# Kernel optimization log

Measured on AMD Instinct MI355X. Metric: run time of the kernel, lower is better.

The kernel has to match this reference:

```python
import jax, jax.numpy as jnp
import numpy as np

DIM = 512
HEADS = 8


def setup_inputs() -> dict:
    key = jax.random.key(0)
    k1, k2, k3, k4 = jax.random.split(key, 4)
    head_dim = DIM // HEADS
    scale = head_dim ** -0.5
    x = jax.random.normal(k1, (4, 4096, DIM), dtype=jnp.float32)
    Wqkv = jax.random.normal(k2, (3 * DIM, DIM), dtype=jnp.float32) * (DIM ** -0.5)
    temperature = jnp.ones((HEADS, 1, 1), dtype=jnp.float32) * scale
    Wproj = jax.random.normal(k3, (DIM, DIM), dtype=jnp.float32) * (DIM ** -0.5)
    bproj = jnp.zeros((DIM,), dtype=jnp.float32)
    return {"x": x, "Wqkv": Wqkv, "temperature": temperature, "Wproj": Wproj, "bproj": bproj}


def reference(x, Wqkv, temperature, Wproj, bproj):
    B, N, C = x.shape
    H = temperature.shape[0]
    D = C // H
    qkv = (x @ Wqkv.T).reshape(B, N, 3, H, D).transpose(2, 0, 3, 1, 4)  # (3,B,H,N,D)
    q, k, v = qkv[0], qkv[1], qkv[2]
    q = jax.nn.relu(q)
    k = jax.nn.relu(k)
    # denom = clamp(q @ sum_n k, min=100) -> (B,H,N,1)
    ksum = k.sum(axis=2)  # (B,H,D)
    denom = jnp.clip(jnp.einsum('bhnd,bhd->bhn', q, ksum), 100.0)[..., None]
    # attn = (k^T v) * temperature -> (B,H,D,D)
    attn = jnp.einsum('bhnd,bhne->bhde', k, v) * temperature
    attn1 = jnp.einsum('bhnd,bhde->bhne', q, attn)  # (B,H,N,D)
    out = attn1 / denom
    y = out.transpose(0, 2, 1, 3).reshape(B, N, C) @ Wproj.T + bproj
    return (y, attn1)
```

## Files before the change

### kernel.cpp

```cpp
#include <hip/hip_runtime.h>
#include <cstdint>
#include <cstddef>

typedef _Float16 f16;
typedef _Float16 f16x4 __attribute__((ext_vector_type(4)));
typedef _Float16 f16x8 __attribute__((ext_vector_type(8)));
typedef float f32x4 __attribute__((ext_vector_type(4)));
typedef __fp16 h2 __attribute__((ext_vector_type(2)));

#define MFMA16(a, b, c) __builtin_amdgcn_mfma_f32_16x16x32_f16(a, b, c, 0, 0, 0)

static __device__ __forceinline__ void gld16(const void* g, void* l) {
  __builtin_amdgcn_global_load_lds(
      (const __attribute__((address_space(1))) void*)g,
      (__attribute__((address_space(3))) void*)l, 16, 0, 0);
}

static __device__ __forceinline__ h2 as_h2(uint32_t u) {
  union { uint32_t u; h2 h; } c; c.u = u; return c.h;
}

#define B_ 4
#define N_ 4096
#define C_ 512
#define H_ 8
#define D_ 64
#define BN_ROWS 16384
#define QKV_COLS 1536

__global__ __launch_bounds__(256) void k_convert(
    const float* __restrict__ x, const float* __restrict__ wqkv,
    const float* __restrict__ wproj,
    f16* __restrict__ xh, f16* __restrict__ wqkvh, f16* __restrict__ wprojh)
{
  const int NX  = (BN_ROWS * C_) / 4;
  const int NW1 = (QKV_COLS * C_) / 4;
  const int NW2 = (C_ * C_) / 4;
  const int total = NX + NW1 + NW2;
  const int stride = gridDim.x * blockDim.x;
  for (int i = blockIdx.x * blockDim.x + threadIdx.x; i < total; i += stride) {
    const float4* s; f16x4* d; int j;
    if (i < NX)              { s = (const float4*)x;     d = (f16x4*)xh;     j = i; }
    else if (i < NX + NW1)   { s = (const float4*)wqkv;  d = (f16x4*)wqkvh;  j = i - NX; }
    else                     { s = (const float4*)wproj; d = (f16x4*)wprojh; j = i - NX - NW1; }
    float4 v = s[j];
    f16x4 o; o[0] = (f16)v.x; o[1] = (f16)v.y; o[2] = (f16)v.z; o[3] = (f16)v.w;
    d[j] = o;
  }
}

__global__ __launch_bounds__(256) void k_qkv_gemm(
    const f16* __restrict__ X, const f16* __restrict__ W, f16* __restrict__ Out)
{
  __shared__ f16 As[128][64];
  __shared__ f16 Bs[128][64];
  int w = (blockIdx.x & 7) * 192 + (blockIdx.x >> 3);
  const int n0 = (w % 12) * 128;
  const int m0 = (w / 12) * 128;
  const int tid = threadIdx.x;
  const int wid = tid >> 6;
  const int lane = tid & 63;
  const int lr = lane & 15, lg = lane >> 4;
  const int sr = lane >> 3;
  const int sslot = (lane & 7) ^ sr;
  const int wr = (wid >> 1) * 64, wc = (wid & 1) * 64;
  f32x4 acc[4][4] = {};
  for (int kt = 0; kt < 512; kt += 64) {
#pragma unroll
    for (int i = 0; i < 4; ++i) {
      int chunk = wid * 4 + i;
      int row = chunk * 8 + sr;
      gld16(&X[(size_t)(m0 + row) * 512 + kt + sslot * 8], &As[chunk * 8][0]);
      gld16(&W[(size_t)(n0 + row) * 512 + kt + sslot * 8], &Bs[chunk * 8][0]);
    }
    __syncthreads();
#pragma unroll
    for (int kk = 0; kk < 2; ++kk) {
      f16x8 af[4], bf[4];
#pragma unroll
      for (int m = 0; m < 4; ++m)
        af[m] = *(const f16x8*)&As[wr + m * 16 + lr][(((kk * 4 + lg) ^ (lr & 7)) * 8)];
#pragma unroll
      for (int n = 0; n < 4; ++n)
        bf[n] = *(const f16x8*)&Bs[wc + n * 16 + lr][(((kk * 4 + lg) ^ (lr & 7)) * 8)];
#pragma unroll
      for (int m = 0; m < 4; ++m)
#pragma unroll
        for (int n = 0; n < 4; ++n)
          acc[m][n] = MFMA16(bf[n], af[m], acc[m][n]);
    }
    __syncthreads();
  }
#pragma unroll
  for (int m = 0; m < 4; ++m)
#pragma unroll
    for (int n = 0; n < 4; ++n) {
      int row = m0 + wr + m * 16 + lr;
      int col = n0 + wc + n * 16 + lg * 4;
      f16x4 o;
      bool relu = (col < 1024);
#pragma unroll
      for (int j = 0; j < 4; ++j) {
        float v = acc[m][n][j];
        if (relu) v = fmaxf(v, 0.f);
        o[j] = (f16)v;
      }
      *(f16x4*)&Out[(size_t)row * QKV_COLS + col] = o;
    }
}

__global__ __launch_bounds__(256) void k_ktv(
    const f16* __restrict__ qkv, float* __restrict__ partial, float* __restrict__ pksum)
{
  __shared__ f16 ks[32][64];
  __shared__ f16 vs[32][64];
  const int bh = blockIdx.x, sp = blockIdx.y;
  const int b = bh >> 3, h = bh & 7;
  const int tid = threadIdx.x, wid = tid >> 6, lane = tid & 63;
  const int srow = lane >> 3, scol = (lane & 7) * 8;
  const int td = (wid << 2) | (lane >> 4);
  const int te = lane & 15;
  const uint32_t SEL_LO = 0x05040100u, SEL_HI = 0x07060302u;
  const h2 ones = {(__fp16)1.0f, (__fp16)1.0f};
  float acc[4][4] = {};
  float ksacc[4] = {0.f, 0.f, 0.f, 0.f};
  const size_t rowbase = (size_t)b * N_ + sp * 256;
  for (int t = 0; t < 8; ++t) {
    int nb = t * 32 + wid * 8 + srow;
    gld16(&qkv[(rowbase + nb) * QKV_COLS + 512 + h * 64 + scol], &ks[wid * 8][0]);
    gld16(&qkv[(rowbase + nb) * QKV_COLS + 1024 + h * 64 + scol], &vs[wid * 8][0]);
    __syncthreads();
#pragma unroll 4
    for (int n = 0; n < 32; n += 2) {
      uint2 ka = *(const uint2*)&ks[n][td * 4];
      uint2 kb = *(const uint2*)&ks[n + 1][td * 4];
      uint2 va = *(const uint2*)&vs[n][te * 4];
      uint2 vb = *(const uint2*)&vs[n + 1][te * 4];
      uint32_t kp[4], vp[4];
      kp[0] = __builtin_amdgcn_perm(kb.x, ka.x, SEL_LO);
      kp[1] = __builtin_amdgcn_perm(kb.x, ka.x, SEL_HI);
      kp[2] = __builtin_amdgcn_perm(kb.y, ka.y, SEL_LO);
      kp[3] = __builtin_amdgcn_perm(kb.y, ka.y, SEL_HI);
      vp[0] = __builtin_amdgcn_perm(vb.x, va.x, SEL_LO);
      vp[1] = __builtin_amdgcn_perm(vb.x, va.x, SEL_HI);
      vp[2] = __builtin_amdgcn_perm(vb.y, va.y, SEL_LO);
      vp[3] = __builtin_amdgcn_perm(vb.y, va.y, SEL_HI);
#pragma unroll
      for (int i = 0; i < 4; ++i)
#pragma unroll
        for (int j = 0; j < 4; ++j)
          acc[i][j] = __builtin_amdgcn_fdot2(as_h2(kp[i]), as_h2(vp[j]), acc[i][j], false);
      if (te == 0) {
#pragma unroll
        for (int i = 0; i < 4; ++i)
          ksacc[i] = __builtin_amdgcn_fdot2(as_h2(kp[i]), ones, ksacc[i], false);
      }
    }
    __syncthreads();
  }
  float* pp = partial + (size_t)(bh * 16 + sp) * 4096;
#pragma unroll
  for (int i = 0; i < 4; ++i)
#pragma unroll
    for (int j = 0; j < 4; ++j)
      pp[(td * 4 + i) * 64 + te * 4 + j] = acc[i][j];
  if (te == 0) {
    float* kp2 = pksum + (bh * 16 + sp) * 64;
#pragma unroll
    for (int i = 0; i < 4; ++i) kp2[td * 4 + i] = ksacc[i];
  }
}

__global__ __launch_bounds__(256) void k_reduce(
    const float* __restrict__ partial, const float* __restrict__ pksum,
    float* __restrict__ attn_acc, float* __restrict__ ksum)
{
  const int bh = blockIdx.x, seg = blockIdx.y, tid = threadIdx.x;
  const int i = seg * 256 + tid;
  float s = 0.f;
#pragma unroll 8
  for (int sp = 0; sp < 16; ++sp) s += partial[(size_t)(bh * 16 + sp) * 4096 + i];
  attn_acc[bh * 4096 + i] = s;
  if (seg == 0 && tid < 64) {
    float t2 = 0.f;
#pragma unroll 8
    for (int sp = 0; sp < 16; ++sp) t2 += pksum[(bh * 16 + sp) * 64 + tid];
    ksum[bh * 64 + tid] = t2;
  }
}

__global__ __launch_bounds__(512, 1) void k_attn_proj(
    const f16* __restrict__ qkv, const float* __restrict__ attn_acc,
    const float* __restrict__ ksum, const float* __restrict__ temp,
    const f16* __restrict__ Wp, const float* __restrict__ bias,
    float* __restrict__ attn1_out, float* __restrict__ Y)
{
  __shared__ f16 outs[8][64][64];
  __shared__ union {
    f16 attnT[8][64][64];
    f16 Bs[512][64];
  } u;
  __shared__ float ksum_s[512];
  __shared__ float bias_s[512];
  __shared__ float denom_s[8][64];

  const int bid = blockIdx.x;
  const int b = bid >> 6, sp = bid & 63;
  const size_t gr = (size_t)b * N_ + sp * 64;
  const int tid = threadIdx.x;
  const int wid = tid >> 6, lane = tid & 63;
  const int lr = lane & 15, lg = lane >> 4;
  const int sr = lane >> 3, sslot = (lane & 7) ^ sr;

  ksum_s[tid] = ksum[b * 512 + tid];
  bias_s[tid] = bias[tid];
  __syncthreads();

  {
    const int h = wid;
    const float tsc = temp[h];
#pragma unroll
    for (int rr = 0; rr < 8; ++rr)
      gld16(&qkv[(gr + rr * 8 + sr) * QKV_COLS + h * 64 + sslot * 8],
            &outs[h][rr * 8][0]);
#pragma unroll
    for (int dc = 0; dc < 4; ++dc) {
      float vals[16];
#pragma unroll
      for (int x = 0; x < 16; ++x)
        vals[x] = attn_acc[(size_t)(b * 8 + h) * 4096 + (dc * 16 + x) * 64 + lane] * tsc;
#pragma unroll
      for (int half = 0; half < 2; ++half) {
        int slot = (dc * 2 + half) ^ (lane & 7);
        f16x8 pk;
#pragma unroll
        for (int j = 0; j < 8; ++j) pk[j] = (f16)vals[half * 8 + j];
        *(f16x8*)&u.attnT[h][lane][slot * 8] = pk;
      }
    }
    asm volatile("s_waitcnt vmcnt(0)" ::: "memory");
    {
      const int r = lane;
      float dot = 0.f;
#pragma unroll
      for (int c = 0; c < 8; ++c) {
        f16x8 qv = *(const f16x8*)&outs[h][r][((c ^ (r & 7)) * 8)];
#pragma unroll
        for (int j = 0; j < 8; ++j) dot += (float)qv[j] * ksum_s[h * 64 + c * 8 + j];
      }
      denom_s[h][r] = fmaxf(dot, 100.f);
    }
    f16x8 af[2][4], bf[4][2];
#pragma unroll
    for (int kk = 0; kk < 2; ++kk)
#pragma unroll
      for (int m = 0; m < 4; ++m)
        af[kk][m] = *(const f16x8*)&outs[h][m * 16 + lr][(((kk * 4 + lg) ^ (lr & 7)) * 8)];
#pragma unroll
    for (int et = 0; et < 4; ++et)
#pragma unroll
      for (int kk = 0; kk < 2; ++kk)
        bf[et][kk] = *(const f16x8*)&u.attnT[h][et * 16 + lr][(((kk * 4 + lg) ^ (lr & 7)) * 8)];
    f32x4 acc1[4][4] = {};
#pragma unroll
    for (int kk = 0; kk < 2; ++kk)
#pragma unroll
      for (int m = 0; m < 4; ++m)
#pragma unroll
        for (int et = 0; et < 4; ++et)
          acc1[m][et] = MFMA16(bf[et][kk], af[kk][m], acc1[m][et]);
#pragma unroll
    for (int m = 0; m < 4; ++m) {
      const int rl = m * 16 + lr;
      const float dn = denom_s[h][rl];
#pragma unroll
      for (int et = 0; et < 4; ++et) {
        int e = et * 16 + lg * 4;
        float4 o;
        o.x = acc1[m][et][0]; o.y = acc1[m][et][1]; o.z = acc1[m][et][2]; o.w = acc1[m][et][3];
        *(float4*)&attn1_out[((size_t)(b * 8 + h) * N_ + sp * 64 + rl) * 64 + e] = o;
        f16x4 oh;
#pragma unroll
        for (int j = 0; j < 4; ++j) oh[j] = (f16)(acc1[m][et][j] / dn);
        *(f16x4*)((char*)&outs[h][rl][0] + (((e >> 3) ^ (rl & 7)) * 16) + (lg & 1) * 8) = oh;
      }
    }
  }
  __syncthreads();

  f32x4 accP[4][4] = {};
  for (int kc = 0; kc < 8; ++kc) {
#pragma unroll
    for (int rd = 0; rd < 8; ++rd)
      gld16(&Wp[(size_t)(wid * 64 + rd * 8 + sr) * 512 + kc * 64 + sslot * 8],
            &u.Bs[wid * 64 + rd * 8][0]);
    __syncthreads();
    f16x8 afp[2][4];
#pragma unroll
    for (int kk = 0; kk < 2; ++kk)
#pragma unroll
      for (int m = 0; m < 4; ++m)
        afp[kk][m] = *(const f16x8*)&outs[kc][m * 16 + lr][(((kk * 4 + lg) ^ (lr & 7)) * 8)];
#pragma unroll
    for (int kk = 0; kk < 2; ++kk) {
      f16x8 bfp[4];
#pragma unroll
      for (int n = 0; n < 4; ++n)
        bfp[n] = *(const f16x8*)&u.Bs[wid * 64 + n * 16 + lr][(((kk * 4 + lg) ^ (lr & 7)) * 8)];
#pragma unroll
      for (int m = 0; m < 4; ++m)
#pragma unroll
        for (int n = 0; n < 4; ++n)
          accP[m][n] = MFMA16(bfp[n], afp[kk][m], accP[m][n]);
    }
    __syncthreads();
  }

#pragma unroll
  for (int m = 0; m < 4; ++m)
#pragma unroll
    for (int n = 0; n < 4; ++n) {
      size_t row = gr + m * 16 + lr;
      int col = wid * 64 + n * 16 + lg * 4;
      float4 o;
      o.x = accP[m][n][0] + bias_s[col + 0];
      o.y = accP[m][n][1] + bias_s[col + 1];
      o.z = accP[m][n][2] + bias_s[col + 2];
      o.w = accP[m][n][3] + bias_s[col + 3];
      *(float4*)&Y[row * C_ + col] = o;
    }
}

extern "C" void kernel_launch(void* const* d_in, const int* in_sizes, int n_in,
                              void* d_out, int out_size, void* d_ws, size_t ws_size,
                              hipStream_t stream)
{
  const float* x     = (const float*)d_in[0];
  const float* wqkv  = (const float*)d_in[1];
  const float* temp  = (const float*)d_in[2];
  const float* wproj = (const float*)d_in[3];
  const float* bproj = (const float*)d_in[4];
  float* y_out     = (float*)d_out;
  float* attn1_out = (float*)d_out + 8388608;

  char* ws = (char*)d_ws;
  f16*   xh       = (f16*)(ws);
  float* partial  = (float*)(ws);
  f16*   wqkvh    = (f16*)(ws + 16777216);
  f16*   wprojh   = (f16*)(ws + 18350080);
  f16*   qkvh     = (f16*)(ws + 18874368);
  float* attn_acc = (float*)(ws + 69206016);
  float* ksum     = (float*)(ws + 69730304);
  float* pksum    = (float*)(ws + 69738496);

  hipLaunchKernelGGL(k_convert,   dim3(2048),   dim3(256), 0, stream, x, wqkv, wproj, xh, wqkvh, wprojh);
  hipLaunchKernelGGL(k_qkv_gemm,  dim3(1536),   dim3(256), 0, stream, xh, wqkvh, qkvh);
  hipLaunchKernelGGL(k_ktv,       dim3(32, 16), dim3(256), 0, stream, qkvh, partial, pksum);
  hipLaunchKernelGGL(k_reduce,    dim3(32, 16), dim3(256), 0, stream, partial, pksum, attn_acc, ksum);
  hipLaunchKernelGGL(k_attn_proj, dim3(256),    dim3(512), 0, stream,
                     qkvh, attn_acc, ksum, temp, wprojh, bproj, attn1_out, y_out);
}
```

Measured before the change: 107.4 us.

## Prefetch per-wave Wproj tiles early and drop block barriers in projection loop

The projection GEMM's Wproj tile loads now target LDS regions that only the issuing wave reads, so the per-iteration __syncthreads pairs become per-wave vmcnt/lgkmcnt waits. The next k-chunk is prefetched right after the current fragments are in registers. The first chunk is staged before the attn1 MFMAs, reusing the wave's own attnT slot in the union. s_setprio is raised around the MFMA bursts. This is meant to hide global-load latency and barrier stalls, but it depends on exact LDS aliasing and hand-placed waitcnts.

```diff
diff --git a/kernel.cpp b/kernel.cpp
--- a/kernel.cpp
+++ b/kernel.cpp
@@ -216,6 +216,14 @@
   bias_s[tid] = bias[tid];
   __syncthreads();
 
+#define STAGEPB(kc_)                                                          \
+  do {                                                                        \
+    _Pragma("unroll")                                                         \
+    for (int rd = 0; rd < 8; ++rd)                                            \
+      gld16(&Wp[(size_t)(wid * 64 + rd * 8 + sr) * 512 + (kc_) * 64 + sslot * 8], \
+            &u.Bs[wid * 64 + rd * 8][0]);                                     \
+  } while (0)
+
   {
     const int h = wid;
     const float tsc = temp[h];
@@ -261,7 +269,11 @@
 #pragma unroll
       for (int kk = 0; kk < 2; ++kk)
         bf[et][kk] = *(const f16x8*)&u.attnT[h][et * 16 + lr][(((kk * 4 + lg) ^ (lr & 7)) * 8)];
+    asm volatile("s_waitcnt lgkmcnt(0)" ::: "memory");
+    __builtin_amdgcn_sched_barrier(0);
+    STAGEPB(0);
     f32x4 acc1[4][4] = {};
+    __builtin_amdgcn_s_setprio(1);
 #pragma unroll
     for (int kk = 0; kk < 2; ++kk)
 #pragma unroll
@@ -269,6 +281,7 @@
 #pragma unroll
         for (int et = 0; et < 4; ++et)
           acc1[m][et] = MFMA16(bf[et][kk], af[kk][m], acc1[m][et]);
+    __builtin_amdgcn_s_setprio(0);
 #pragma unroll
     for (int m = 0; m < 4; ++m) {
       const int rl = m * 16 + lr;
@@ -286,35 +299,38 @@
       }
     }
   }
-  __syncthreads();
+  asm volatile("s_waitcnt lgkmcnt(0)" ::: "memory");
+  __builtin_amdgcn_s_barrier();
+  asm volatile("" ::: "memory");
 
   f32x4 accP[4][4] = {};
+#pragma unroll
   for (int kc = 0; kc < 8; ++kc) {
-#pragma unroll
-    for (int rd = 0; rd < 8; ++rd)
-      gld16(&Wp[(size_t)(wid * 64 + rd * 8 + sr) * 512 + kc * 64 + sslot * 8],
-            &u.Bs[wid * 64 + rd * 8][0]);
-    __syncthreads();
-    f16x8 afp[2][4];
+    asm volatile("s_waitcnt vmcnt(0)" ::: "memory");
+    f16x8 bfp[2][4], afp[2][4];
+#pragma unroll
+    for (int kk = 0; kk < 2; ++kk) {
+#pragma unroll
+      for (int n = 0; n < 4; ++n)
+        bfp[kk][n] = *(const f16x8*)&u.Bs[wid * 64 + n * 16 + lr][(((kk * 4 + lg) ^ (lr & 7)) * 8)];
+#pragma unroll
+      for (int m = 0; m < 4; ++m)
+        afp[kk][m] = *(const f16x8*)&outs[kc][m * 16 + lr][(((kk * 4 + lg) ^ (lr & 7)) * 8)];
+    }
+    asm volatile("s_waitcnt lgkmcnt(0)" ::: "memory");
+    __builtin_amdgcn_sched_barrier(0);
+    if (kc < 7) STAGEPB(kc + 1);
+    __builtin_amdgcn_s_setprio(1);
 #pragma unroll
     for (int kk = 0; kk < 2; ++kk)
 #pragma unroll
       for (int m = 0; m < 4; ++m)
-        afp[kk][m] = *(const f16x8*)&outs[kc][m * 16 + lr][(((kk * 4 + lg) ^ (lr & 7)) * 8)];
-#pragma unroll
-    for (int kk = 0; kk < 2; ++kk) {
-      f16x8 bfp[4];
-#pragma unroll
-      for (int n = 0; n < 4; ++n)
-        bfp[n] = *(const f16x8*)&u.Bs[wid * 64 + n * 16 + lr][(((kk * 4 + lg) ^ (lr & 7)) * 8)];
-#pragma unroll
-      for (int m = 0; m < 4; ++m)
 #pragma unroll
         for (int n = 0; n < 4; ++n)
-          accP[m][n] = MFMA16(bfp[n], afp[kk][m], accP[m][n]);
-    }
-    __syncthreads();
-  }
+          accP[m][n] = MFMA16(bfp[kk][n], afp[kk][m], accP[m][n]);
+    __builtin_amdgcn_s_setprio(0);
+  }
+#undef STAGEPB
 
 #pragma unroll
   for (int m = 0; m < 4; ++m)
```

New measurement: 103.7 us, median of 2. 1.04x faster.
